# Performance work log

Measured on AMD Instinct MI355X. Metric: run time of the kernel, lower is better.

## Reference

```python
import math
import jax, jax.numpy as jnp
import numpy as np

D = 256      # embedding_dim (= internal_dim, downsample_rate 1)
H = 8        # num_heads
HD = D // H  # head_dim = 32
NTC = 16     # num_text_classes
NIMG = 4096  # image tokens (64x64)
N = NIMG + NTC
B = 2
NKE = 64     # num_k_exclude_rope


def _rope(x, freqs):
    # x: (b, h, n, c); freqs: (n, c//2, 2) = (cos, sin) of complex rotary factors
    b, h, n, c = x.shape
    xp = x.reshape(b, h, n, c // 2, 2)
    cos, sin = freqs[..., 0], freqs[..., 1]
    xr, xi = xp[..., 0], xp[..., 1]
    out_r = xr * cos - xi * sin
    out_i = xr * sin + xi * cos
    return jnp.stack([out_r, out_i], axis=-1).reshape(b, h, n, c)


def _sep_heads(x):
    b, n, c = x.shape
    return x.reshape(b, n, H, c // H).transpose(0, 2, 1, 3)  # (b,h,n,hd)


def setup_inputs() -> dict:
    key = jax.random.key(0)
    ks = jax.random.split(key, 14)
    s = 0.02
    # rotary factors: unit-norm cos/sin pairs
    ang_img = jax.random.uniform(ks[3], (NIMG, HD // 2)) * (2.0 * np.pi)
    ang_txt = jax.random.uniform(ks[4], (NTC, HD // 2)) * (2.0 * np.pi)
    return {
        "q": jax.random.normal(ks[0], (B, N, D), dtype=jnp.float32),
        "k": jax.random.normal(ks[1], (B, N, D), dtype=jnp.float32),
        "v": jax.random.normal(ks[2], (B, N, D), dtype=jnp.float32),
        "freqs_cis_img": jnp.stack([jnp.cos(ang_img), jnp.sin(ang_img)], axis=-1),
        "freqs_cis_txt": jnp.stack([jnp.cos(ang_txt), jnp.sin(ang_txt)], axis=-1),
        "Wq": jax.random.normal(ks[5], (D, D), dtype=jnp.float32) * s,
        "bq": jnp.zeros((D,), dtype=jnp.float32),
        "Wk": jax.random.normal(ks[6], (D, D), dtype=jnp.float32) * s,
        "bk": jnp.zeros((D,), dtype=jnp.float32),
        "Wv": jax.random.normal(ks[7], (D, D), dtype=jnp.float32) * s,
        "bv": jnp.zeros((D,), dtype=jnp.float32),
        "Wo": jax.random.normal(ks[8], (D, D), dtype=jnp.float32) * s,
        "bo": jnp.zeros((D,), dtype=jnp.float32),
        "num_k_exclude_rope": NKE,
    }


def reference(q, k, v, freqs_cis_img, freqs_cis_txt,
              Wq, bq, Wk, bk, Wv, bv, Wo, bo, num_k_exclude_rope):
    q = q @ Wq.T + bq
    k = k @ Wk.T + bk
    v = v @ Wv.T + bv
    q = _sep_heads(q)  # (b,h,n,hd)
    k = _sep_heads(k)
    v = _sep_heads(v)

    # split tokens into image / text regions, apply RoPE separately
    q_img, q_txt = q[:, :, :-NTC, :], q[:, :, -NTC:, :]
    k_img, k_txt = k[:, :, :-NTC, :], k[:, :, -NTC:, :]
    q_img = _rope(q_img, freqs_cis_img)
    k_img = _rope(k_img, freqs_cis_img)
    q_txt = _rope(q_txt, freqs_cis_txt)
    k_txt = _rope(k_txt, freqs_cis_txt)
    q = jnp.concatenate([q_img, q_txt], axis=-2)
    k = jnp.concatenate([k_img, k_txt], axis=-2)

    scale = 1.0 / math.sqrt(HD)
    nke = num_k_exclude_rope
    if nke > 0:
        k_td, k_mem = k[:, :, :-nke, :], k[:, :, -nke:, :]
        v_td, v_mem = v[:, :, :-nke, :], v[:, :, -nke:, :]
        attn = jax.nn.softmax(jnp.einsum('bhqd,bhkd->bhqk', q, k_td) * scale, axis=-1)
        out = jnp.einsum('bhqk,bhkd->bhqd', attn, v_td)
        attn_m = jax.nn.softmax(jnp.einsum('bhqd,bhkd->bhqk', q, k_mem) * scale, axis=-1)
        out = out + jnp.einsum('bhqk,bhkd->bhqd', attn_m, v_mem)
    else:
        attn = jax.nn.softmax(jnp.einsum('bhqd,bhkd->bhqk', q, k) * scale, axis=-1)
        out = jnp.einsum('bhqk,bhkd->bhqd', attn, v)

    b, h, n, hd = out.shape
    out = out.transpose(0, 2, 1, 3).reshape(b, n, h * hd)
    return out @ Wo.T + bo
```

## Files before the change

### kernel.cpp

```cpp
#include <hip/hip_runtime.h>
#include <hip/hip_bf16.h>

#define BN    4112
#define NKR   4160
#define BNP   4160
#define BB    2
#define HH    8
#define NIMG_ 4096
#define NMAIN 4048
#define MROWS 8224
#define QSCALE 0.25505402f

typedef __attribute__((ext_vector_type(8))) short short8;
typedef __attribute__((ext_vector_type(4))) float f32x4;
typedef __attribute__((ext_vector_type(16))) float f32x16;

__device__ __forceinline__ unsigned short f2bs(float x) { return __bfloat16_as_ushort(__float2bfloat16(x)); }
__device__ __forceinline__ unsigned pkbf(float a, float b) {
    __hip_bfloat162 h = __float22bfloat162_rn(make_float2(a, b));
    unsigned u; __builtin_memcpy(&u, &h, 4); return u;
}
__device__ __forceinline__ float fexp2(float x) {
#if __has_builtin(__builtin_amdgcn_exp2f)
    return __builtin_amdgcn_exp2f(x);
#else
    return exp2f(x);
#endif
}

__global__ __launch_bounds__(256)
void qkv_mfma(const float* __restrict__ Aq, const float* __restrict__ Ak, const float* __restrict__ Av,
              const float* __restrict__ Wq, const float* __restrict__ Wk, const float* __restrict__ Wv,
              const float* __restrict__ bq, const float* __restrict__ bk, const float* __restrict__ bv,
              short* __restrict__ Qr, short* __restrict__ Kr, short* __restrict__ Vt,
              const float* __restrict__ fimg, const float* __restrict__ ftxt)
{
    __shared__ __align__(16) short Ws[2][64][72];
    __shared__ __align__(16) short Ds[2][64][72];

    const int mode = blockIdx.z;
    const float* A    = (mode == 0) ? Aq : (mode == 1) ? Ak : Av;
    const float* W    = (mode == 0) ? Wq : (mode == 1) ? Wk : Wv;
    const float* bias = (mode == 0) ? bq : (mode == 1) ? bk : bv;

    const int t    = threadIdx.x;
    const int wave = t >> 6, lane = t & 63, q16 = lane & 15, quad = lane >> 4;
    const int f0 = blockIdx.x * 64;
    const int m0 = blockIdx.y * 64;
    const int sr = t >> 2, sc = (t & 3) * 16;
    const int arow = m0 + sr;
    const bool aval = arow < MROWS;
    const float* wp = W + (size_t)(f0 + sr) * 256 + sc;
    const float* ap = A + (size_t)(aval ? arow : 0) * 256 + sc;

    f32x4 acc[4] = {{0,0,0,0},{0,0,0,0},{0,0,0,0},{0,0,0,0}};

    uint4 wr0, wr1, dr0, dr1;
    {
        float4 a0 = *(const float4*)(wp),     a1 = *(const float4*)(wp + 4);
        float4 a2 = *(const float4*)(wp + 8), a3 = *(const float4*)(wp + 12);
        wr0 = uint4{pkbf(a0.x,a0.y), pkbf(a0.z,a0.w), pkbf(a1.x,a1.y), pkbf(a1.z,a1.w)};
        wr1 = uint4{pkbf(a2.x,a2.y), pkbf(a2.z,a2.w), pkbf(a3.x,a3.y), pkbf(a3.z,a3.w)};
        a0 = *(const float4*)(ap);     a1 = *(const float4*)(ap + 4);
        a2 = *(const float4*)(ap + 8); a3 = *(const float4*)(ap + 12);
        dr0 = uint4{pkbf(a0.x,a0.y), pkbf(a0.z,a0.w), pkbf(a1.x,a1.y), pkbf(a1.z,a1.w)};
        dr1 = uint4{pkbf(a2.x,a2.y), pkbf(a2.z,a2.w), pkbf(a3.x,a3.y), pkbf(a3.z,a3.w)};
    }
    *(uint4*)&Ws[0][sr][sc] = wr0; *(uint4*)&Ws[0][sr][sc + 8] = wr1;
    *(uint4*)&Ds[0][sr][sc] = dr0; *(uint4*)&Ds[0][sr][sc + 8] = dr1;
    __syncthreads();

    #pragma unroll
    for (int ki = 0; ki < 4; ++ki) {
        const int buf = ki & 1;
        if (ki < 3) {
            const int k1 = (ki + 1) * 64;
            float4 a0 = *(const float4*)(wp + k1),     a1 = *(const float4*)(wp + k1 + 4);
            float4 a2 = *(const float4*)(wp + k1 + 8), a3 = *(const float4*)(wp + k1 + 12);
            wr0 = uint4{pkbf(a0.x,a0.y), pkbf(a0.z,a0.w), pkbf(a1.x,a1.y), pkbf(a1.z,a1.w)};
            wr1 = uint4{pkbf(a2.x,a2.y), pkbf(a2.z,a2.w), pkbf(a3.x,a3.y), pkbf(a3.z,a3.w)};
            a0 = *(const float4*)(ap + k1);     a1 = *(const float4*)(ap + k1 + 4);
            a2 = *(const float4*)(ap + k1 + 8); a3 = *(const float4*)(ap + k1 + 12);
            dr0 = uint4{pkbf(a0.x,a0.y), pkbf(a0.z,a0.w), pkbf(a1.x,a1.y), pkbf(a1.z,a1.w)};
            dr1 = uint4{pkbf(a2.x,a2.y), pkbf(a2.z,a2.w), pkbf(a3.x,a3.y), pkbf(a3.z,a3.w)};
        }
        #pragma unroll
        for (int ks = 0; ks < 2; ++ks) {
            const short8 af = *(const short8*)&Ws[buf][wave * 16 + q16][ks * 32 + quad * 8];
            #pragma unroll
            for (int ct = 0; ct < 4; ++ct) {
                const short8 bf = *(const short8*)&Ds[buf][ct * 16 + q16][ks * 32 + quad * 8];
                acc[ct] = __builtin_amdgcn_mfma_f32_16x16x32_bf16(af, bf, acc[ct], 0, 0, 0);
            }
        }
        if (ki < 3) {
            *(uint4*)&Ws[buf ^ 1][sr][sc] = wr0; *(uint4*)&Ws[buf ^ 1][sr][sc + 8] = wr1;
            *(uint4*)&Ds[buf ^ 1][sr][sc] = dr0; *(uint4*)&Ds[buf ^ 1][sr][sc + 8] = dr1;
            __syncthreads();
        }
    }

    const int fbase = f0 + wave * 16 + quad * 4;
    const float4 bb = *(const float4*)(bias + fbase);
    float vs[4][4];
    #pragma unroll
    for (int ct = 0; ct < 4; ++ct) {
        int n = m0 + ct * 16 + q16;
        float v0 = acc[ct][0] + bb.x, v1 = acc[ct][1] + bb.y;
        float v2 = acc[ct][2] + bb.z, v3 = acc[ct][3] + bb.w;
        int b  = (n >= BN) ? 1 : 0;
        int nb = n - b * BN;
        if (mode < 2) {
            int j0 = (fbase & 31) >> 1;
            const float* fr = (nb < NIMG_) ? (fimg + ((size_t)nb * 16 + j0) * 2)
                                           : (ftxt + ((size_t)(nb - NIMG_) * 16 + j0) * 2);
            float4 cs = *(const float4*)fr;
            float r0 = v0 * cs.x - v1 * cs.y, i0 = v0 * cs.y + v1 * cs.x;
            float r1 = v2 * cs.z - v3 * cs.w, i1 = v2 * cs.w + v3 * cs.z;
            v0 = r0; v1 = i0; v2 = r1; v3 = i1;
        }
        if (mode == 2) {
            vs[ct][0] = v0; vs[ct][1] = v1; vs[ct][2] = v2; vs[ct][3] = v3;
            continue;
        }
        if (n >= MROWS) continue;
        const int h = (fbase >> 5) & 7, hd = fbase & 31;
        if (mode == 0) {
            unsigned short* op = (unsigned short*)Qr + (((size_t)(b * HH + h) * BN + nb) * 32 + hd);
            *(uint2*)op = uint2{pkbf(v0 * QSCALE, v1 * QSCALE), pkbf(v2 * QSCALE, v3 * QSCALE)};
        } else {
            int nk = nb + ((nb >= NMAIN) ? 48 : 0);
            unsigned short* op = (unsigned short*)Kr + (((size_t)(b * HH + h) * NKR + nk) * 32 + hd);
            *(uint2*)op = uint2{pkbf(v0, v1), pkbf(v2, v3)};
        }
    }

    if (mode == 2) {
        short (*Tr)[72] = Ds[0];
        const int fl = wave * 16 + quad * 4;
        #pragma unroll
        for (int ct = 0; ct < 4; ++ct) {
            const int nl = ct * 16 + q16;
            Tr[fl + 0][nl] = (short)f2bs(vs[ct][0]);
            Tr[fl + 1][nl] = (short)f2bs(vs[ct][1]);
            Tr[fl + 2][nl] = (short)f2bs(vs[ct][2]);
            Tr[fl + 3][nl] = (short)f2bs(vs[ct][3]);
        }
        __syncthreads();
        const int h0 = (f0 >> 5) & 7;
        #pragma unroll
        for (int ii = 0; ii < 2; ++ii) {
            const int r  = ii * 32 + (t >> 3);
            const int c8 = (t & 7) * 8;
            const int ng = m0 + c8;
            if (ng < MROWS) {
                uint4 val = *(const uint4*)&Tr[r][c8];
                int b  = (ng >= BN) ? 1 : 0;
                int nb = ng - b * BN;
                int nk = nb + ((nb >= NMAIN) ? 48 : 0);
                int h  = h0 + (r >> 5), hd = r & 31;
                unsigned short* op = (unsigned short*)Vt + ((size_t)(b * HH + h) * 32 + hd) * BNP + nk;
                *(uint4*)op = val;
            }
        }
    }

    if (blockIdx.x == 0 && blockIdx.y < 16 && t < 192) {
        const int bh = blockIdx.y;
        if (mode == 1) {
            short* base = Kr + (size_t)bh * NKR * 32 + (size_t)NMAIN * 32;
            *(uint4*)(base + t * 8) = uint4{0u, 0u, 0u, 0u};
        } else if (mode == 2) {
            short* base = Vt + (size_t)bh * 32 * BNP + (size_t)(t / 6) * BNP + NMAIN + (t % 6) * 8;
            *(uint4*)base = uint4{0u, 0u, 0u, 0u};
        }
    }
}

__global__ __launch_bounds__(512, 4)
void attn_mfma(const short* __restrict__ Qr, const short* __restrict__ Kr,
               const short* __restrict__ Vt, unsigned short* __restrict__ AO)
{
    __shared__ __align__(16) short Ks[2][2][64][40];
    __shared__ __align__(16) short Vs[2][2][32][72];

    const int t    = threadIdx.x;
    const int wave = t >> 6, lane = t & 63, q32 = lane & 31, hi = lane >> 5;
    const int grp  = wave >> 2, w4 = wave & 3;
    const int bh = blockIdx.y;
    const int q  = blockIdx.x * 128 + w4 * 32 + q32;
    const int qc = (q < BN) ? q : (BN - 1);
    const short* qp = Qr + ((size_t)bh * BN + qc) * 32 + hi * 8;
    const short8 qf0 = *(const short8*)(qp);
    const short8 qf1 = *(const short8*)(qp + 16);

    f32x16 oA = {0,0,0,0,0,0,0,0,0,0,0,0,0,0,0,0};
    f32x16 oB = {0,0,0,0,0,0,0,0,0,0,0,0,0,0,0,0};
    const f32x16 z16 = {0,0,0,0,0,0,0,0,0,0,0,0,0,0,0,0};
    float LA = 0.f, LB = 0.f;

    const int tg = t & 255;
    const int kr = tg >> 2, kc = tg & 3;
    const int vr = tg >> 3, vc = tg & 7;
    const short* kg = Kr + (size_t)bh * NKR * 32 + (size_t)grp * 65536 + (size_t)kr * 32 + kc * 8;
    const short* vg = Vt + (size_t)bh * 32 * BNP + (size_t)vr * BNP + grp * 2048
                         + (vc >> 1) * 16 + (vc & 1) * 4;
    const int ntiles = 32 + grp;

    auto tile = [&](int buf, f32x16& o, float& L) {
        float lsum = 0.f;
        #pragma unroll
        for (int h = 0; h < 2; ++h) {
            const short8 kf0 = *(const short8*)&Ks[grp][buf][h * 32 + q32][hi * 8];
            const short8 kf1 = *(const short8*)&Ks[grp][buf][h * 32 + q32][16 + hi * 8];
            f32x16 s = __builtin_amdgcn_mfma_f32_32x32x16_bf16(kf0, qf0, z16, 0, 0, 0);
            s = __builtin_amdgcn_mfma_f32_32x32x16_bf16(kf1, qf1, s, 0, 0, 0);
            float p[16];
            #pragma unroll
            for (int r = 0; r < 16; ++r) p[r] = fexp2(s[r]);
            lsum += (((p[0]+p[1])+(p[2]+p[3])) + ((p[4]+p[5])+(p[6]+p[7])))
                  + (((p[8]+p[9])+(p[10]+p[11])) + ((p[12]+p[13])+(p[14]+p[15])));
            #pragma unroll
            for (int m = 0; m < 2; ++m) {
                uint4 pbu = uint4{pkbf(p[8*m+0], p[8*m+1]), pkbf(p[8*m+2], p[8*m+3]),
                                  pkbf(p[8*m+4], p[8*m+5]), pkbf(p[8*m+6], p[8*m+7])};
                short8 pb; __builtin_memcpy(&pb, &pbu, 16);
                const short8 vf = *(const short8*)&Vs[grp][buf][q32][h * 32 + m * 16 + hi * 8];
                o = __builtin_amdgcn_mfma_f32_32x32x16_bf16(vf, pb, o, 0, 0, 0);
            }
        }
        L += lsum;
    };

    *(uint4*)&Ks[grp][0][kr][kc * 8] = *(const uint4*)(kg);
    {
        uint2 va = *(const uint2*)(vg);
        uint2 vb = *(const uint2*)(vg + 8);
        *(uint4*)&Vs[grp][0][vr][vc * 8] = uint4{va.x, va.y, vb.x, vb.y};
    }
    __syncthreads();

    for (int it = 0; it < 33; ++it) {
        const int buf = it & 1;
        uint4 kreg; uint2 vreg0, vreg1;
        const bool pre = (it + 1) < ntiles;
        if (pre) {
            kreg  = *(const uint4*)(kg + (size_t)(it + 1) * 2048);
            vreg0 = *(const uint2*)(vg + (it + 1) * 64);
            vreg1 = *(const uint2*)(vg + (it + 1) * 64 + 8);
        }
        if (it < ntiles) {
            __builtin_amdgcn_s_setprio(1);
            if (grp == 0)      tile(buf, oA, LA);
            else if (it < 32)  tile(buf, oA, LA);
            else               tile(buf, oB, LB);
            __builtin_amdgcn_s_setprio(0);
        }
        if (pre) {
            *(uint4*)&Ks[grp][buf ^ 1][kr][kc * 8] = kreg;
            *(uint4*)&Vs[grp][buf ^ 1][vr][vc * 8] = uint4{vreg0.x, vreg0.y, vreg1.x, vreg1.y};
        }
        __syncthreads();
    }

    LA += __shfl_xor(LA, 32);
    LB += __shfl_xor(LB, 32);

    float* ex = (float*)&Ks[0][0][0][0];
    const int slot = (w4 * 64 + lane) * 20;
    if (grp == 0) {
        #pragma unroll
        for (int i = 0; i < 4; ++i)
            *(f32x4*)(ex + slot + 4 * i) = f32x4{oA[4*i], oA[4*i+1], oA[4*i+2], oA[4*i+3]};
        ex[slot + 16] = LA;
    }
    __syncthreads();

    if (grp == 1 && q < BN) {
        float LT = LA + ex[slot + 16] - 48.f;
        const float iA = 1.f / LT, iB = 1.f / LB;
        const int b = bh >> 3, h = bh & 7;
        unsigned short* ap = AO + ((size_t)b * BN + q) * 256 + h * 32;
        #pragma unroll
        for (int k = 0; k < 4; ++k) {
            f32x4 a = *(const f32x4*)(ex + slot + 4 * k);
            float w0 = (oA[4*k+0] + a[0]) * iA + oB[4*k+0] * iB;
            float w1 = (oA[4*k+1] + a[1]) * iA + oB[4*k+1] * iB;
            float w2 = (oA[4*k+2] + a[2]) * iA + oB[4*k+2] * iB;
            float w3 = (oA[4*k+3] + a[3]) * iA + oB[4*k+3] * iB;
            *(uint2*)(ap + 8 * k + 4 * hi) = uint2{pkbf(w0, w1), pkbf(w2, w3)};
        }
    }
}

__global__ __launch_bounds__(256)
void gemm_out(const unsigned short* __restrict__ A, const float* __restrict__ W,
              const float* __restrict__ bias, float* __restrict__ out)
{
    __shared__ __align__(16) short Ws[2][64][72];
    __shared__ __align__(16) short Ds[2][64][72];
    const int t    = threadIdx.x;
    const int wave = t >> 6, lane = t & 63, q16 = lane & 15, quad = lane >> 4;
    const int f0 = blockIdx.x * 64, m0 = blockIdx.y * 64;
    const int sr = t >> 2, sc = (t & 3) * 16;
    const int arow = m0 + sr;
    const bool aval = arow < MROWS;
    const float* wp = W + (size_t)(f0 + sr) * 256 + sc;
    const unsigned short* ap = A + (size_t)(aval ? arow : 0) * 256 + sc;

    f32x4 acc[4] = {{0,0,0,0},{0,0,0,0},{0,0,0,0},{0,0,0,0}};

    uint4 wr0, wr1, dr0, dr1;
    {
        float4 a0 = *(const float4*)(wp),     a1 = *(const float4*)(wp + 4);
        float4 a2 = *(const float4*)(wp + 8), a3 = *(const float4*)(wp + 12);
        wr0 = uint4{pkbf(a0.x,a0.y), pkbf(a0.z,a0.w), pkbf(a1.x,a1.y), pkbf(a1.z,a1.w)};
        wr1 = uint4{pkbf(a2.x,a2.y), pkbf(a2.z,a2.w), pkbf(a3.x,a3.y), pkbf(a3.z,a3.w)};
        dr0 = *(const uint4*)(ap); dr1 = *(const uint4*)(ap + 8);
    }
    *(uint4*)&Ws[0][sr][sc] = wr0; *(uint4*)&Ws[0][sr][sc + 8] = wr1;
    *(uint4*)&Ds[0][sr][sc] = dr0; *(uint4*)&Ds[0][sr][sc + 8] = dr1;
    __syncthreads();

    #pragma unroll
    for (int ki = 0; ki < 4; ++ki) {
        const int buf = ki & 1;
        if (ki < 3) {
            const int k1 = (ki + 1) * 64;
            float4 a0 = *(const float4*)(wp + k1),     a1 = *(const float4*)(wp + k1 + 4);
            float4 a2 = *(const float4*)(wp + k1 + 8), a3 = *(const float4*)(wp + k1 + 12);
            wr0 = uint4{pkbf(a0.x,a0.y), pkbf(a0.z,a0.w), pkbf(a1.x,a1.y), pkbf(a1.z,a1.w)};
            wr1 = uint4{pkbf(a2.x,a2.y), pkbf(a2.z,a2.w), pkbf(a3.x,a3.y), pkbf(a3.z,a3.w)};
            dr0 = *(const uint4*)(ap + k1); dr1 = *(const uint4*)(ap + k1 + 8);
        }
        #pragma unroll
        for (int ks = 0; ks < 2; ++ks) {
            const short8 af = *(const short8*)&Ws[buf][wave * 16 + q16][ks * 32 + quad * 8];
            #pragma unroll
            for (int ct = 0; ct < 4; ++ct) {
                const short8 bf = *(const short8*)&Ds[buf][ct * 16 + q16][ks * 32 + quad * 8];
                acc[ct] = __builtin_amdgcn_mfma_f32_16x16x32_bf16(af, bf, acc[ct], 0, 0, 0);
            }
        }
        if (ki < 3) {
            *(uint4*)&Ws[buf ^ 1][sr][sc] = wr0; *(uint4*)&Ws[buf ^ 1][sr][sc + 8] = wr1;
            *(uint4*)&Ds[buf ^ 1][sr][sc] = dr0; *(uint4*)&Ds[buf ^ 1][sr][sc + 8] = dr1;
            __syncthreads();
        }
    }

    const int fbase = f0 + wave * 16 + quad * 4;
    const float4 bb = *(const float4*)(bias + fbase);
    #pragma unroll
    for (int ct = 0; ct < 4; ++ct) {
        int n = m0 + ct * 16 + q16;
        if (n >= MROWS) continue;
        float* op = out + (size_t)n * 256 + fbase;
        *(float4*)op = float4{acc[ct][0] + bb.x, acc[ct][1] + bb.y,
                              acc[ct][2] + bb.z, acc[ct][3] + bb.w};
    }
}

extern "C" void kernel_launch(void* const* d_in, const int* in_sizes, int n_in,
                              void* d_out, int out_size, void* d_ws, size_t ws_size,
                              hipStream_t stream)
{
    (void)in_sizes; (void)n_in; (void)out_size; (void)ws_size;
    const float* q    = (const float*)d_in[0];
    const float* k    = (const float*)d_in[1];
    const float* v    = (const float*)d_in[2];
    const float* fimg = (const float*)d_in[3];
    const float* ftxt = (const float*)d_in[4];
    const float* Wq   = (const float*)d_in[5];
    const float* bq   = (const float*)d_in[6];
    const float* Wk   = (const float*)d_in[7];
    const float* bk   = (const float*)d_in[8];
    const float* Wv   = (const float*)d_in[9];
    const float* bv   = (const float*)d_in[10];
    const float* Wo   = (const float*)d_in[11];
    const float* bo   = (const float*)d_in[12];

    char* w = (char*)d_ws;
    short*          Qr = (short*)(w);
    short*          Kr = (short*)(w + 4210688);
    short*          Vt = (short*)(w + 8470528);
    unsigned short* AO = (unsigned short*)(w + 12730368);

    qkv_mfma<<<dim3(4, 129, 3), 256, 0, stream>>>(q, k, v, Wq, Wk, Wv, bq, bk, bv,
                                                  Qr, Kr, Vt, fimg, ftxt);
    attn_mfma<<<dim3(33, 16), 512, 0, stream>>>(Qr, Kr, Vt, AO);
    gemm_out<<<dim3(4, 129), 256, 0, stream>>>(AO, Wo, bo, (float*)d_out);
}
```

Measured before the change: 205.4 us.

## Halve attention block size and interleave two independent score MFMA chains

The attention kernel now uses 256-thread blocks with 64 queries each instead of 512-thread blocks with 128 queries, roughly doubling the grid so work spreads more evenly across CUs. Each thread now loads twice as much K/V per tile so the shared-memory tiles are still fully filled. The tile routine computes both 32-key halves' score MFMAs back to back and accumulates into two separate output accumulators, which breaks the serial MFMA dependency chain and exposes more instruction-level parallelism. The cost is that each K/V tile is reused by only half as many queries, so global and L2 traffic for K/V roughly doubles, and the extra accumulator raises register pressure.

```diff
diff --git a/kernel.cpp b/kernel.cpp
--- a/kernel.cpp
+++ b/kernel.cpp
@@ -177,7 +177,7 @@
     }
 }
 
-__global__ __launch_bounds__(512, 4)
+__global__ __launch_bounds__(256, 4)
 void attn_mfma(const short* __restrict__ Qr, const short* __restrict__ Kr,
                const short* __restrict__ Vt, unsigned short* __restrict__ AO)
 {
@@ -186,20 +186,21 @@
 
     const int t    = threadIdx.x;
     const int wave = t >> 6, lane = t & 63, q32 = lane & 31, hi = lane >> 5;
-    const int grp  = wave >> 2, w4 = wave & 3;
+    const int grp  = wave >> 1, w2 = wave & 1;
     const int bh = blockIdx.y;
-    const int q  = blockIdx.x * 128 + w4 * 32 + q32;
+    const int q  = blockIdx.x * 64 + w2 * 32 + q32;
     const int qc = (q < BN) ? q : (BN - 1);
     const short* qp = Qr + ((size_t)bh * BN + qc) * 32 + hi * 8;
     const short8 qf0 = *(const short8*)(qp);
     const short8 qf1 = *(const short8*)(qp + 16);
 
-    f32x16 oA = {0,0,0,0,0,0,0,0,0,0,0,0,0,0,0,0};
-    f32x16 oB = {0,0,0,0,0,0,0,0,0,0,0,0,0,0,0,0};
+    f32x16 oAx = {0,0,0,0,0,0,0,0,0,0,0,0,0,0,0,0};
+    f32x16 oAy = {0,0,0,0,0,0,0,0,0,0,0,0,0,0,0,0};
+    f32x16 oBx = {0,0,0,0,0,0,0,0,0,0,0,0,0,0,0,0};
     const f32x16 z16 = {0,0,0,0,0,0,0,0,0,0,0,0,0,0,0,0};
     float LA = 0.f, LB = 0.f;
 
-    const int tg = t & 255;
+    const int tg = t & 127;
     const int kr = tg >> 2, kc = tg & 3;
     const int vr = tg >> 3, vc = tg & 7;
     const short* kg = Kr + (size_t)bh * NKR * 32 + (size_t)grp * 65536 + (size_t)kr * 32 + kc * 8;
@@ -207,67 +208,89 @@
                          + (vc >> 1) * 16 + (vc & 1) * 4;
     const int ntiles = 32 + grp;
 
-    auto tile = [&](int buf, f32x16& o, float& L) {
-        float lsum = 0.f;
-        #pragma unroll
-        for (int h = 0; h < 2; ++h) {
-            const short8 kf0 = *(const short8*)&Ks[grp][buf][h * 32 + q32][hi * 8];
-            const short8 kf1 = *(const short8*)&Ks[grp][buf][h * 32 + q32][16 + hi * 8];
-            f32x16 s = __builtin_amdgcn_mfma_f32_32x32x16_bf16(kf0, qf0, z16, 0, 0, 0);
-            s = __builtin_amdgcn_mfma_f32_32x32x16_bf16(kf1, qf1, s, 0, 0, 0);
-            float p[16];
-            #pragma unroll
-            for (int r = 0; r < 16; ++r) p[r] = fexp2(s[r]);
-            lsum += (((p[0]+p[1])+(p[2]+p[3])) + ((p[4]+p[5])+(p[6]+p[7])))
-                  + (((p[8]+p[9])+(p[10]+p[11])) + ((p[12]+p[13])+(p[14]+p[15])));
-            #pragma unroll
-            for (int m = 0; m < 2; ++m) {
-                uint4 pbu = uint4{pkbf(p[8*m+0], p[8*m+1]), pkbf(p[8*m+2], p[8*m+3]),
-                                  pkbf(p[8*m+4], p[8*m+5]), pkbf(p[8*m+6], p[8*m+7])};
-                short8 pb; __builtin_memcpy(&pb, &pbu, 16);
-                const short8 vf = *(const short8*)&Vs[grp][buf][q32][h * 32 + m * 16 + hi * 8];
-                o = __builtin_amdgcn_mfma_f32_32x32x16_bf16(vf, pb, o, 0, 0, 0);
-            }
-        }
-        L += lsum;
+    auto tile = [&](int buf, f32x16& ox, f32x16& oy, float& L) {
+        const short8 kf00 = *(const short8*)&Ks[grp][buf][q32][hi * 8];
+        const short8 kf01 = *(const short8*)&Ks[grp][buf][q32][16 + hi * 8];
+        const short8 kf10 = *(const short8*)&Ks[grp][buf][32 + q32][hi * 8];
+        const short8 kf11 = *(const short8*)&Ks[grp][buf][32 + q32][16 + hi * 8];
+        f32x16 s0 = __builtin_amdgcn_mfma_f32_32x32x16_bf16(kf00, qf0, z16, 0, 0, 0);
+        f32x16 s1 = __builtin_amdgcn_mfma_f32_32x32x16_bf16(kf10, qf0, z16, 0, 0, 0);
+        s0 = __builtin_amdgcn_mfma_f32_32x32x16_bf16(kf01, qf1, s0, 0, 0, 0);
+        s1 = __builtin_amdgcn_mfma_f32_32x32x16_bf16(kf11, qf1, s1, 0, 0, 0);
+        float p0[16], p1[16];
+        #pragma unroll
+        for (int r = 0; r < 16; ++r) p0[r] = fexp2(s0[r]);
+        #pragma unroll
+        for (int r = 0; r < 16; ++r) p1[r] = fexp2(s1[r]);
+        float l0 = (((p0[0]+p0[1])+(p0[2]+p0[3])) + ((p0[4]+p0[5])+(p0[6]+p0[7])))
+                 + (((p0[8]+p0[9])+(p0[10]+p0[11])) + ((p0[12]+p0[13])+(p0[14]+p0[15])));
+        float l1 = (((p1[0]+p1[1])+(p1[2]+p1[3])) + ((p1[4]+p1[5])+(p1[6]+p1[7])))
+                 + (((p1[8]+p1[9])+(p1[10]+p1[11])) + ((p1[12]+p1[13])+(p1[14]+p1[15])));
+        #pragma unroll
+        for (int m = 0; m < 2; ++m) {
+            uint4 pbu = uint4{pkbf(p0[8*m+0], p0[8*m+1]), pkbf(p0[8*m+2], p0[8*m+3]),
+                              pkbf(p0[8*m+4], p0[8*m+5]), pkbf(p0[8*m+6], p0[8*m+7])};
+            short8 pb; __builtin_memcpy(&pb, &pbu, 16);
+            const short8 vf = *(const short8*)&Vs[grp][buf][q32][m * 16 + hi * 8];
+            ox = __builtin_amdgcn_mfma_f32_32x32x16_bf16(vf, pb, ox, 0, 0, 0);
+        }
+        #pragma unroll
+        for (int m = 0; m < 2; ++m) {
+            uint4 pbu = uint4{pkbf(p1[8*m+0], p1[8*m+1]), pkbf(p1[8*m+2], p1[8*m+3]),
+                              pkbf(p1[8*m+4], p1[8*m+5]), pkbf(p1[8*m+6], p1[8*m+7])};
+            short8 pb; __builtin_memcpy(&pb, &pbu, 16);
+            const short8 vf = *(const short8*)&Vs[grp][buf][q32][32 + m * 16 + hi * 8];
+            oy = __builtin_amdgcn_mfma_f32_32x32x16_bf16(vf, pb, oy, 0, 0, 0);
+        }
+        L += l0 + l1;
     };
 
-    *(uint4*)&Ks[grp][0][kr][kc * 8] = *(const uint4*)(kg);
+    *(uint4*)&Ks[grp][0][kr][kc * 8]      = *(const uint4*)(kg);
+    *(uint4*)&Ks[grp][0][kr + 32][kc * 8] = *(const uint4*)(kg + 1024);
     {
-        uint2 va = *(const uint2*)(vg);
-        uint2 vb = *(const uint2*)(vg + 8);
-        *(uint4*)&Vs[grp][0][vr][vc * 8] = uint4{va.x, va.y, vb.x, vb.y};
+        uint2 a0 = *(const uint2*)(vg),              b0 = *(const uint2*)(vg + 8);
+        uint2 a1 = *(const uint2*)(vg + 16 * BNP),   b1 = *(const uint2*)(vg + 16 * BNP + 8);
+        *(uint4*)&Vs[grp][0][vr][vc * 8]      = uint4{a0.x, a0.y, b0.x, b0.y};
+        *(uint4*)&Vs[grp][0][vr + 16][vc * 8] = uint4{a1.x, a1.y, b1.x, b1.y};
     }
     __syncthreads();
 
     for (int it = 0; it < 33; ++it) {
         const int buf = it & 1;
-        uint4 kreg; uint2 vreg0, vreg1;
+        uint4 kreg0, kreg1; uint2 va0, vb0, va1, vb1;
         const bool pre = (it + 1) < ntiles;
         if (pre) {
-            kreg  = *(const uint4*)(kg + (size_t)(it + 1) * 2048);
-            vreg0 = *(const uint2*)(vg + (it + 1) * 64);
-            vreg1 = *(const uint2*)(vg + (it + 1) * 64 + 8);
+            const short* kp = kg + (size_t)(it + 1) * 2048;
+            kreg0 = *(const uint4*)(kp);
+            kreg1 = *(const uint4*)(kp + 1024);
+            const short* vp = vg + (it + 1) * 64;
+            va0 = *(const uint2*)(vp);            vb0 = *(const uint2*)(vp + 8);
+            va1 = *(const uint2*)(vp + 16 * BNP); vb1 = *(const uint2*)(vp + 16 * BNP + 8);
         }
         if (it < ntiles) {
             __builtin_amdgcn_s_setprio(1);
-            if (grp == 0)      tile(buf, oA, LA);
-            else if (it < 32)  tile(buf, oA, LA);
-            else               tile(buf, oB, LB);
+            if (grp == 0)      tile(buf, oAx, oAy, LA);
+            else if (it < 32)  tile(buf, oAx, oAy, LA);
+            else               tile(buf, oBx, oBx, LB);
             __builtin_amdgcn_s_setprio(0);
         }
         if (pre) {
-            *(uint4*)&Ks[grp][buf ^ 1][kr][kc * 8] = kreg;
-            *(uint4*)&Vs[grp][buf ^ 1][vr][vc * 8] = uint4{vreg0.x, vreg0.y, vreg1.x, vreg1.y};
+            *(uint4*)&Ks[grp][buf ^ 1][kr][kc * 8]      = kreg0;
+            *(uint4*)&Ks[grp][buf ^ 1][kr + 32][kc * 8] = kreg1;
+            *(uint4*)&Vs[grp][buf ^ 1][vr][vc * 8]      = uint4{va0.x, va0.y, vb0.x, vb0.y};
+            *(uint4*)&Vs[grp][buf ^ 1][vr + 16][vc * 8] = uint4{va1.x, va1.y, vb1.x, vb1.y};
         }
         __syncthreads();
     }
+
+    f32x16 oA = oAx + oAy;
+    f32x16 oB = oBx;
 
     LA += __shfl_xor(LA, 32);
     LB += __shfl_xor(LB, 32);
 
     float* ex = (float*)&Ks[0][0][0][0];
-    const int slot = (w4 * 64 + lane) * 20;
+    const int slot = (w2 * 64 + lane) * 20;
     if (grp == 0) {
         #pragma unroll
         for (int i = 0; i < 4; ++i)
@@ -388,6 +411,6 @@
 
     qkv_mfma<<<dim3(4, 129, 3), 256, 0, stream>>>(q, k, v, Wq, Wk, Wv, bq, bk, bv,
                                                   Qr, Kr, Vt, fimg, ftxt);
-    attn_mfma<<<dim3(33, 16), 512, 0, stream>>>(Qr, Kr, Vt, AO);
+    attn_mfma<<<dim3(65, 16), 256, 0, stream>>>(Qr, Kr, Vt, AO);
     gemm_out<<<dim3(4, 129), 256, 0, stream>>>(AO, Wo, bo, (float*)d_out);
 }
```

Result: no change. 202.2 us (-1.6%).
